# Performance work log

Hardware: AMD Instinct MI355X
Metric: run time of the kernel (lower is better)

## Reference

```python
import jax, jax.numpy as jnp
import numpy as np

N_NODES = 10000
N_EDGES = 640000
D_NODE = 128
D_EDGE = 64
D_IN = D_NODE + D_EDGE  # 192
D_OUT = 128


def setup_inputs() -> dict:
    key = jax.random.key(0)
    k1, k2, k3, k4 = jax.random.split(key, 4)
    x = jax.random.normal(k1, (N_NODES, D_NODE), dtype=jnp.float32)
    edge_index = jax.random.randint(k2, (2, N_EDGES), 0, N_NODES, dtype=jnp.int64)
    edge_features = jax.random.normal(k3, (N_EDGES, D_EDGE), dtype=jnp.float32)
    W = jax.random.normal(k4, (D_IN, D_OUT), dtype=jnp.float32) * (1.0 / np.sqrt(D_IN))
    b = jnp.zeros((D_OUT,), dtype=jnp.float32)
    return {"x": x, "edge_index": edge_index, "edge_features": edge_features, "W": W, "b": b}


def reference(x, edge_index, edge_features, W, b):
    n_nodes = x.shape[0]
    src = edge_index[0]  # [E]
    dst = edge_index[1]  # [E]
    # gather source node feats, concat edge feats, linear
    h = jnp.concatenate([x[src], edge_features], axis=1)  # [E, D_IN]
    h = h @ W + b  # [E, D_OUT]
    # scatter-mean to destination nodes
    sums = jax.ops.segment_sum(h, dst, num_segments=n_nodes)  # [N, D_OUT]
    cnt = jax.ops.segment_sum(jnp.ones((h.shape[0],), dtype=h.dtype), dst, num_segments=n_nodes)
    return sums / jnp.maximum(cnt, 1.0)[:, None]
```

## Files before the change

### kernel.cpp

```cpp
#include <hip/hip_runtime.h>

#define D_NODE 128
#define D_EDGE 64
#define D_IN 192
#define D_OUT 128


__global__ void k_hist(const int* __restrict__ dst, int* __restrict__ cnt, int E) {
    int i = blockIdx.x * 256 + threadIdx.x;
    int e = i * 4;
    if (e + 4 <= E) {
        int4 d = *(const int4*)(dst + e);
        atomicAdd(&cnt[d.x], 1);
        atomicAdd(&cnt[d.y], 1);
        atomicAdd(&cnt[d.z], 1);
        atomicAdd(&cnt[d.w], 1);
    } else {
        for (; e < E; ++e) atomicAdd(&cnt[dst[e]], 1);
    }
}

__global__ __launch_bounds__(1024) void k_scan(const int* __restrict__ cnt,
                                               int* __restrict__ offsets,
                                               int* __restrict__ cursor, int N) {
    __shared__ int wsum[16];
    int tid = threadIdx.x;
    int lane = tid & 63, wid = tid >> 6;
    const int CH = (N + 1023) / 1024;
    int i0 = tid * CH;
    int local[16];
    int lsum = 0;
    for (int c = 0; c < CH; ++c) {
        int i = i0 + c;
        int v = (i < N) ? cnt[i] : 0;
        local[c] = v;
        lsum += v;
    }
    int incl = lsum;
    for (int off = 1; off < 64; off <<= 1) {
        int t = __shfl_up(incl, off, 64);
        if (lane >= off) incl += t;
    }
    if (lane == 63) wsum[wid] = incl;
    __syncthreads();
    if (wid == 0) {
        int s = (lane < 16) ? wsum[lane] : 0;
        for (int off = 1; off < 16; off <<= 1) {
            int t = __shfl_up(s, off, 64);
            if (lane >= off) s += t;
        }
        if (lane < 16) wsum[lane] = s;
    }
    __syncthreads();
    int waveoff = (wid > 0) ? wsum[wid - 1] : 0;
    int run = waveoff + incl - lsum;
    for (int c = 0; c < CH; ++c) {
        int i = i0 + c;
        if (i < N) { offsets[i] = run; cursor[i] = run; run += local[c]; }
    }
    if (tid == 0) offsets[N] = wsum[15];
}

__global__ void k_scatter(const int* __restrict__ ei, int* __restrict__ cursor,
                          int2* __restrict__ csr, int E) {
    int e = blockIdx.x * 256 + threadIdx.x;
    if (e < E) {
        int s = ei[e];
        int d = ei[E + e];
        int pos = atomicAdd(&cursor[d], 1);
        csr[pos] = make_int2(s, e);
    }
}

__global__ __launch_bounds__(256) void k_gather(
        const float2* __restrict__ x2, const float* __restrict__ ef,
        const int* __restrict__ offsets, const int2* __restrict__ csr,
        float* __restrict__ agg, int N) {
    int wid = threadIdx.x >> 6;
    int lane = threadIdx.x & 63;
    int node = blockIdx.x * 4 + wid;
    if (node >= N) return;
    int start = offsets[node];
    int end = offsets[node + 1];
    float ax[4] = {0.f, 0.f, 0.f, 0.f};
    float ay[4] = {0.f, 0.f, 0.f, 0.f};
    float az[4] = {0.f, 0.f, 0.f, 0.f};
    for (int base = start; base < end; base += 64) {
        int m = end - base;
        if (m > 64) m = 64;
        int2 ent = make_int2(0, 0);
        if (lane < m) ent = csr[base + lane];
        int j = 0;
        for (; j + 8 <= m; j += 8) {
            float2 xv[8];
            float  ev[8];
#pragma unroll
            for (int u = 0; u < 8; ++u) {
                int s  = __shfl(ent.x, j + u, 64);
                int id = __shfl(ent.y, j + u, 64);
                xv[u] = x2[(unsigned)s * 64u + lane];
                ev[u] = ef[(unsigned)id * 64u + lane];
            }
#pragma unroll
            for (int u = 0; u < 8; ++u) {
                ax[u & 3] += xv[u].x;
                ay[u & 3] += xv[u].y;
                az[u & 3] += ev[u];
            }
        }
        for (; j < m; ++j) {
            int s  = __shfl(ent.x, j, 64);
            int id = __shfl(ent.y, j, 64);
            float2 xv = x2[(unsigned)s * 64u + lane];
            float  ev = ef[(unsigned)id * 64u + lane];
            ax[0] += xv.x; ay[0] += xv.y; az[0] += ev;
        }
    }
    float a0 = (ax[0] + ax[1]) + (ax[2] + ax[3]);
    float a1 = (ay[0] + ay[1]) + (ay[2] + ay[3]);
    float a2 = (az[0] + az[1]) + (az[2] + az[3]);
    float2* aggrow = (float2*)(agg + (size_t)node * D_IN);
    aggrow[lane] = make_float2(a0, a1);
    agg[(size_t)node * D_IN + 128 + lane] = a2;
}

__global__ __launch_bounds__(256) void k_gemm(
        const float* __restrict__ agg, const float* __restrict__ W,
        const float* __restrict__ b, const int* __restrict__ offsets,
        float* __restrict__ out, int N) {
    __shared__ float sAgg[16][D_IN];
    __shared__ int scnt[16];
    int tid = threadIdx.x;
    int n0 = blockIdx.x * 16;
    for (int i = tid; i < 16 * D_IN; i += 256) {
        int m = i / D_IN;
        int k = i - m * D_IN;
        int n = n0 + m;
        sAgg[m][k] = (n < N) ? agg[(size_t)n * D_IN + k] : 0.0f;
    }
    if (tid < 16) {
        int n = n0 + tid;
        scnt[tid] = (n < N) ? (offsets[n + 1] - offsets[n]) : 0;
    }
    __syncthreads();
    int o = tid & 127;
    int g = tid >> 7;
    float acc[8];
#pragma unroll
    for (int m = 0; m < 8; ++m) acc[m] = 0.0f;
    for (int k = 0; k < D_IN; k += 4) {
        float w0 = W[(k + 0) * D_OUT + o];
        float w1 = W[(k + 1) * D_OUT + o];
        float w2 = W[(k + 2) * D_OUT + o];
        float w3 = W[(k + 3) * D_OUT + o];
#pragma unroll
        for (int m = 0; m < 8; ++m) {
            const float4 av = *(const float4*)(&sAgg[g * 8 + m][k]);
            acc[m] += av.x * w0 + av.y * w1 + av.z * w2 + av.w * w3;
        }
    }
    float bo = b[o];
#pragma unroll
    for (int m = 0; m < 8; ++m) {
        int n = n0 + g * 8 + m;
        if (n < N) {
            int c = scnt[g * 8 + m];
            out[(size_t)n * D_OUT + o] = (c > 0) ? (acc[m] / (float)c + bo) : 0.0f;
        }
    }
}

extern "C" void kernel_launch(void* const* d_in, const int* in_sizes, int n_in,
                              void* d_out, int out_size, void* d_ws, size_t ws_size,
                              hipStream_t stream) {
    const float* x  = (const float*)d_in[0];
    const int*   ei = (const int*)d_in[1];
    const float* ef = (const float*)d_in[2];
    const float* W  = (const float*)d_in[3];
    const float* b  = (const float*)d_in[4];
    float* out = (float*)d_out;

    const int N = in_sizes[0] / D_NODE;
    const int E = in_sizes[2] / D_EDGE;

    auto align64 = [](size_t v) { return (v + 63) & ~(size_t)63; };
    char* ws = (char*)d_ws;
    size_t o_cnt = 0;
    size_t o_off = align64(o_cnt + (size_t)N * 4);
    size_t o_cur = align64(o_off + (size_t)(N + 1) * 4);
    size_t o_csr = align64(o_cur + (size_t)N * 4);
    size_t o_agg = align64(o_csr + (size_t)E * 8);
    int*  cnt     = (int*)(ws + o_cnt);
    int*  offsets = (int*)(ws + o_off);
    int*  cursor  = (int*)(ws + o_cur);
    int2* csr     = (int2*)(ws + o_csr);
    float* agg    = (float*)(ws + o_agg);

    hipMemsetAsync(cnt, 0, (size_t)N * 4, stream);
    k_hist<<<(E / 4 + 255) / 256, 256, 0, stream>>>(ei + E, cnt, E);
    k_scan<<<1, 1024, 0, stream>>>(cnt, offsets, cursor, N);
    k_scatter<<<(E + 255) / 256, 256, 0, stream>>>(ei, cursor, csr, E);
    k_gather<<<(N + 3) / 4, 256, 0, stream>>>((const float2*)x, ef, offsets, csr, agg, N);
    k_gemm<<<(N + 15) / 16, 256, 0, stream>>>(agg, W, b, offsets, out, N);
}
```

Measured before the change: 377.5 us.

## Record per-edge rank during histogram to remove second atomic pass in CSR build

The histogram kernel now stores the value returned by each atomicAdd as a per-edge rank, so the placement kernel computes each CSR position as offsets[dst] plus rank without a second round of atomics on a cursor array. The cursor array is dropped and an E-sized rank buffer is added, which costs an extra write and read of E ints. The gather kernel also switches the CSR entry loads and the edge-feature loads to nontemporal loads, to keep streamed data from evicting the reused node features in cache.

```diff
diff --git a/kernel.cpp b/kernel.cpp
--- a/kernel.cpp
+++ b/kernel.cpp
@@ -6,23 +6,14 @@
 #define D_OUT 128
 
 
-__global__ void k_hist(const int* __restrict__ dst, int* __restrict__ cnt, int E) {
-    int i = blockIdx.x * 256 + threadIdx.x;
-    int e = i * 4;
-    if (e + 4 <= E) {
-        int4 d = *(const int4*)(dst + e);
-        atomicAdd(&cnt[d.x], 1);
-        atomicAdd(&cnt[d.y], 1);
-        atomicAdd(&cnt[d.z], 1);
-        atomicAdd(&cnt[d.w], 1);
-    } else {
-        for (; e < E; ++e) atomicAdd(&cnt[dst[e]], 1);
-    }
+__global__ void k_rank(const int* __restrict__ dst, int* __restrict__ cnt,
+                       int* __restrict__ rank, int E) {
+    int e = blockIdx.x * 256 + threadIdx.x;
+    if (e < E) rank[e] = atomicAdd(&cnt[dst[e]], 1);
 }
 
 __global__ __launch_bounds__(1024) void k_scan(const int* __restrict__ cnt,
-                                               int* __restrict__ offsets,
-                                               int* __restrict__ cursor, int N) {
+                                               int* __restrict__ offsets, int N) {
     __shared__ int wsum[16];
     int tid = threadIdx.x;
     int lane = tid & 63, wid = tid >> 6;
@@ -56,19 +47,18 @@
     int run = waveoff + incl - lsum;
     for (int c = 0; c < CH; ++c) {
         int i = i0 + c;
-        if (i < N) { offsets[i] = run; cursor[i] = run; run += local[c]; }
+        if (i < N) { offsets[i] = run; run += local[c]; }
     }
     if (tid == 0) offsets[N] = wsum[15];
 }
 
-__global__ void k_scatter(const int* __restrict__ ei, int* __restrict__ cursor,
-                          int2* __restrict__ csr, int E) {
+__global__ void k_place(const int* __restrict__ ei, const int* __restrict__ offsets,
+                        const int* __restrict__ rank, int2* __restrict__ csr, int E) {
     int e = blockIdx.x * 256 + threadIdx.x;
     if (e < E) {
-        int s = ei[e];
         int d = ei[E + e];
-        int pos = atomicAdd(&cursor[d], 1);
-        csr[pos] = make_int2(s, e);
+        int pos = offsets[d] + rank[e];
+        csr[pos] = make_int2(ei[e], e);
     }
 }
 
@@ -89,7 +79,11 @@
         int m = end - base;
         if (m > 64) m = 64;
         int2 ent = make_int2(0, 0);
-        if (lane < m) ent = csr[base + lane];
+        if (lane < m) {
+            long long raw = __builtin_nontemporal_load((const long long*)(csr + base + lane));
+            ent.x = (int)(raw & 0xffffffffLL);
+            ent.y = (int)(raw >> 32);
+        }
         int j = 0;
         for (; j + 8 <= m; j += 8) {
             float2 xv[8];
@@ -99,7 +93,7 @@
                 int s  = __shfl(ent.x, j + u, 64);
                 int id = __shfl(ent.y, j + u, 64);
                 xv[u] = x2[(unsigned)s * 64u + lane];
-                ev[u] = ef[(unsigned)id * 64u + lane];
+                ev[u] = __builtin_nontemporal_load(ef + (unsigned)id * 64u + lane);
             }
 #pragma unroll
             for (int u = 0; u < 8; ++u) {
@@ -112,7 +106,7 @@
             int s  = __shfl(ent.x, j, 64);
             int id = __shfl(ent.y, j, 64);
             float2 xv = x2[(unsigned)s * 64u + lane];
-            float  ev = ef[(unsigned)id * 64u + lane];
+            float  ev = __builtin_nontemporal_load(ef + (unsigned)id * 64u + lane);
             ax[0] += xv.x; ay[0] += xv.y; az[0] += ev;
         }
     }
@@ -187,19 +181,19 @@
     char* ws = (char*)d_ws;
     size_t o_cnt = 0;
     size_t o_off = align64(o_cnt + (size_t)N * 4);
-    size_t o_cur = align64(o_off + (size_t)(N + 1) * 4);
-    size_t o_csr = align64(o_cur + (size_t)N * 4);
+    size_t o_rnk = align64(o_off + (size_t)(N + 1) * 4);
+    size_t o_csr = align64(o_rnk + (size_t)E * 4);
     size_t o_agg = align64(o_csr + (size_t)E * 8);
     int*  cnt     = (int*)(ws + o_cnt);
     int*  offsets = (int*)(ws + o_off);
-    int*  cursor  = (int*)(ws + o_cur);
+    int*  rank    = (int*)(ws + o_rnk);
     int2* csr     = (int2*)(ws + o_csr);
     float* agg    = (float*)(ws + o_agg);
 
     hipMemsetAsync(cnt, 0, (size_t)N * 4, stream);
-    k_hist<<<(E / 4 + 255) / 256, 256, 0, stream>>>(ei + E, cnt, E);
-    k_scan<<<1, 1024, 0, stream>>>(cnt, offsets, cursor, N);
-    k_scatter<<<(E + 255) / 256, 256, 0, stream>>>(ei, cursor, csr, E);
+    k_rank<<<(E + 255) / 256, 256, 0, stream>>>(ei + E, cnt, rank, E);
+    k_scan<<<1, 1024, 0, stream>>>(cnt, offsets, N);
+    k_place<<<(E + 255) / 256, 256, 0, stream>>>(ei, offsets, rank, csr, E);
     k_gather<<<(N + 3) / 4, 256, 0, stream>>>((const float2*)x, ef, offsets, csr, agg, N);
     k_gemm<<<(N + 15) / 16, 256, 0, stream>>>(agg, W, b, offsets, out, N);
 }
```

After: 341.3 us. -9.6%, faster.
